# Performance work log

Hardware: AMD Instinct MI355X
Metric: run time of the kernel (lower is better)

Reference implementation:

```python
import jax, jax.numpy as jnp
import numpy as np

D = 1024      # in_features
H = 768       # hidden_features per routed expert
E = 8         # n_routed_experts
K = 2         # n_activated_experts
NS = 2        # n_shared_experts
ROUTE_SCALE = 1.0


def setup_inputs() -> dict:
    key = jax.random.key(0)
    ks = jax.random.split(key, 6)
    s = 0.02
    return {
        "x": jax.random.normal(ks[0], (2, 1024, D), jnp.float32),
        "gate_w": jax.random.normal(ks[1], (E, D), jnp.float32) * s,
        "W1": jax.random.normal(ks[2], (E, 2 * H, D), jnp.float32) * s,   # expert fc1 (y|gate)
        "W2": jax.random.normal(ks[3], (E, D, H), jnp.float32) * s,       # expert fc2
        "Ws1": jax.random.normal(ks[4], (2 * NS * H, D), jnp.float32) * s,  # shared fc1
        "Ws2": jax.random.normal(ks[5], (D, NS * H), jnp.float32) * s,      # shared fc2
    }


def _gated_mlp(x, w1, w2):
    # GatedMLP: fc1 -> chunk(2) -> y * silu(gate) -> fc2, all bias-free
    h = x @ w1.T
    y, g = jnp.split(h, 2, axis=-1)
    return (y * jax.nn.silu(g)) @ w2.T


def reference(x, gate_w, W1, W2, Ws1, Ws2):
    x_shape = x.shape
    xf = x.reshape(-1, D)                 # [T, D]
    T = xf.shape[0]

    # --- Gate: softmax scores in fp32, top-k routing ---
    scores = jax.nn.softmax((xf @ gate_w.T).astype(jnp.float32), axis=-1)  # [T, E]
    top_vals, top_idx = jax.lax.top_k(scores, K)
    # no bias branch (in_features != 7168): gathered original scores == top_k values
    weights = (top_vals * ROUTE_SCALE).astype(x.dtype)                      # [T, K]

    # Dense per-token/expert combine weights (0 for unselected experts);
    # mathematically identical to the per-expert gather/scatter-add combine.
    w_dense = jnp.zeros((T, E), x.dtype).at[jnp.arange(T)[:, None], top_idx].set(weights)

    # --- Routed experts (stacked GatedMLPs) ---
    h = jnp.einsum('td,ehd->teh', xf, W1)        # [T, E, 2H]
    y, g = jnp.split(h, 2, axis=-1)
    eo = jnp.einsum('teh,edh->ted', y * jax.nn.silu(g), W2)  # [T, E, D]
    z = jnp.einsum('te,ted->td', w_dense, eo)    # weighted combine

    # --- Shared experts ---
    z = z + _gated_mlp(xf, Ws1, Ws2)
    return z.reshape(x_shape)
```

## Files before the change

### kernel.cpp

```cpp
#include <hip/hip_runtime.h>
#include <hip/hip_bf16.h>


typedef short bf16x8 __attribute__((ext_vector_type(8)));
typedef float f32x4 __attribute__((ext_vector_type(4)));

__device__ __forceinline__ unsigned short f2b(float f) {
    __hip_bfloat16 h = __float2bfloat16(f);
    return *reinterpret_cast<unsigned short*>(&h);
}

__device__ __forceinline__ void ldst16(const unsigned short* g, unsigned short* l) {
    __builtin_amdgcn_global_load_lds(
        (const __attribute__((address_space(1))) unsigned int*)g,
        (__attribute__((address_space(3))) unsigned int*)l, 16, 0, 0);
}

__device__ __forceinline__ void cvt8(const float* s, unsigned short* d, int j) {
    const float4* sp = reinterpret_cast<const float4*>(s) + (size_t)j * 2;
    float4 v0 = sp[0], v1 = sp[1];
    union { unsigned short u[8]; uint4 v; } o;
    o.u[0]=f2b(v0.x); o.u[1]=f2b(v0.y); o.u[2]=f2b(v0.z); o.u[3]=f2b(v0.w);
    o.u[4]=f2b(v1.x); o.u[5]=f2b(v1.y); o.u[6]=f2b(v1.z); o.u[7]=f2b(v1.w);
    *(reinterpret_cast<uint4*>(d) + j) = o.v;
}

__global__ __launch_bounds__(256) void k_convgate(const float* __restrict__ x,
                                                  const float* __restrict__ gw,
                                                  const float* __restrict__ W1,
                                                  const float* __restrict__ Ws1,
                                                  const float* __restrict__ W2,
                                                  const float* __restrict__ Ws2,
                                                  unsigned short* __restrict__ xb,
                                                  unsigned short* __restrict__ W1b,
                                                  unsigned short* __restrict__ Ws1b,
                                                  unsigned short* __restrict__ W2b,
                                                  unsigned short* __restrict__ Ws2b,
                                                  int* __restrict__ tokslot,
                                                  float* __restrict__ wroute,
                                                  int* __restrict__ cnt,
                                                  float* __restrict__ out) {
    __shared__ float red[4][8];
    __shared__ float sc[8];
    const int b = blockIdx.x, tid = threadIdx.x;
    if (b < 11520) {
        int i = b * 256 + tid;
        if (i < 1572864)       cvt8(W1,  W1b,  i);
        else if (i < 1966080)  cvt8(Ws1, Ws1b, i - 1572864);
        else if (i < 2752512)  cvt8(W2,  W2b,  i - 1966080);
        else if (i < 2949120)  cvt8(Ws2, Ws2b, i - 2752512);
        return;
    }
    const int t = b - 11520;
    const int lane = tid & 63, w = tid >> 6;

    float4 v = reinterpret_cast<const float4*>(x + (size_t)t * 1024)[tid];
    union { unsigned short u[4]; } o;
    o.u[0]=f2b(v.x); o.u[1]=f2b(v.y); o.u[2]=f2b(v.z); o.u[3]=f2b(v.w);
    reinterpret_cast<ushort4*>(xb + (size_t)t * 1024)[tid] = *(ushort4*)o.u;

    float p[8];
    for (int e = 0; e < 8; e++) {
        float4 g = reinterpret_cast<const float4*>(gw + (size_t)e * 1024)[tid];
        p[e] = v.x*g.x + v.y*g.y + v.z*g.z + v.w*g.w;
    }
    for (int e = 0; e < 8; e++)
        for (int off = 32; off > 0; off >>= 1) p[e] += __shfl_down(p[e], off, 64);
    if (lane == 0)
        for (int e = 0; e < 8; e++) red[w][e] = p[e];
    __syncthreads();
    if (tid < 8) sc[tid] = red[0][tid] + red[1][tid] + red[2][tid] + red[3][tid];
    __syncthreads();
    if (tid == 0) {
        float m = sc[0];
        for (int e = 1; e < 8; e++) m = fmaxf(m, sc[e]);
        float ex[8], sum = 0.f;
        for (int e = 0; e < 8; e++) { ex[e] = expf(sc[e] - m); sum += ex[e]; }
        float inv = 1.f / sum;
        int i1 = 0;
        for (int e = 1; e < 8; e++) if (sc[e] > sc[i1]) i1 = e;
        int i2 = -1; float s2 = -1e30f;
        for (int e = 0; e < 8; e++) if (e != i1 && sc[e] > s2) { s2 = sc[e]; i2 = e; }
        int p1 = atomicAdd(&cnt[i1 * 16], 1);
        tokslot[i1 * 2048 + p1] = t; wroute[i1 * 2048 + p1] = ex[i1] * inv;
        int p2 = atomicAdd(&cnt[i2 * 16], 1);
        tokslot[i2 * 2048 + p2] = t; wroute[i2 * 2048 + p2] = ex[i2] * inv;
    }
    reinterpret_cast<float4*>(out + (size_t)t * 1024)[tid] = (float4){0.f, 0.f, 0.f, 0.f};
}

__global__ __launch_bounds__(256) void k_fc1u(const unsigned short* __restrict__ xb,
                                              const unsigned short* __restrict__ W1b,
                                              const unsigned short* __restrict__ Ws1b,
                                              const int* __restrict__ tokslot,
                                              const float* __restrict__ wroute,
                                              const int* __restrict__ cnt,
                                              unsigned short* __restrict__ act_r,
                                              unsigned short* __restrict__ acts) {
    __shared__ alignas(16) unsigned short As[128 * 64];
    __shared__ alignas(16) unsigned short Bs[128 * 64];
    const int tid = threadIdx.x, lane = tid & 63, w = tid >> 6;
    const int wr = w >> 1, wc = w & 1;
    const int mt = blockIdx.x / 12, ht = blockIdx.x % 12;

    int pre = 0, sel = -1, base = 0;
    for (int ee = 0; ee < 10; ee++) {
        int til = (ee < 8) ? ((cnt[ee * 16] + 127) >> 7) : 16;
        if (sel < 0 && mt < pre + til) { sel = ee; base = pre; }
        pre += til;
    }
    if (sel < 0) return;
    const int e = sel, m0 = (mt - base) * 128, h0 = ht * 64;
    const int Te = (e < 8) ? cnt[e * 16] : 2048;
    const unsigned short* Bp = (e < 8) ? (W1b + (size_t)e * 1536 * 1024)
                                       : (Ws1b + (size_t)(e - 8) * 768 * 1024);
    const int gOff = (e < 8) ? 768 : 1536;

    const int kc = tid & 7;
    int aoff[4], boff[4];
    for (int q = 0; q < 4; q++) {
        int row = q * 32 + (tid >> 3);
        int idx = m0 + row;
        int tk = (e < 8) ? ((idx < Te) ? tokslot[e * 2048 + idx] : 0) : idx;
        aoff[q] = tk * 1024 + ((kc ^ (row & 7)) << 3);
        int grow = (row < 64) ? (h0 + row) : (gOff + h0 + row - 64);
        boff[q] = grow * 1024 + ((kc ^ (row & 7)) << 3);
    }

    f32x4 accy[4][2], accg[4][2];
    for (int i = 0; i < 4; i++)
        for (int j = 0; j < 2; j++) {
            accy[i][j] = (f32x4){0.f, 0.f, 0.f, 0.f};
            accg[i][j] = (f32x4){0.f, 0.f, 0.f, 0.f};
        }

    for (int k0 = 0; k0 < 1024; k0 += 64) {
        for (int q = 0; q < 4; q++) {
            ldst16(xb + aoff[q] + k0, As + (q * 256 + tid) * 8);
            ldst16(Bp + boff[q] + k0, Bs + (q * 256 + tid) * 8);
        }
        __syncthreads();
        for (int kh = 0; kh < 2; kh++) {
            const int cq = kh * 4 + (lane >> 4);
            bf16x8 a[4], by[2], bg[2];
            for (int i = 0; i < 4; i++) {
                int r = 64 * wr + 16 * i + (lane & 15);
                a[i] = *(const bf16x8*)&As[r * 64 + ((cq ^ (r & 7)) << 3)];
            }
            for (int j = 0; j < 2; j++) {
                int ry = 32 * wc + 16 * j + (lane & 15);
                by[j] = *(const bf16x8*)&Bs[ry * 64 + ((cq ^ (ry & 7)) << 3)];
                int rg = 64 + ry;
                bg[j] = *(const bf16x8*)&Bs[rg * 64 + ((cq ^ (rg & 7)) << 3)];
            }
            for (int i = 0; i < 4; i++)
                for (int j = 0; j < 2; j++) {
                    accy[i][j] = __builtin_amdgcn_mfma_f32_16x16x32_bf16(a[i], by[j], accy[i][j], 0, 0, 0);
                    accg[i][j] = __builtin_amdgcn_mfma_f32_16x16x32_bf16(a[i], bg[j], accg[i][j], 0, 0, 0);
                }
        }
        __syncthreads();
    }

    for (int i = 0; i < 4; i++)
        for (int r = 0; r < 4; r++) {
            int irow = m0 + 64 * wr + 16 * i + ((lane >> 4) << 2) + r;
            if (irow >= Te) continue;
            float sw = (e < 8) ? wroute[e * 2048 + irow] : 1.0f;
            unsigned short* dst = (e < 8)
                ? (act_r + ((size_t)e * 2048 + irow) * 768)
                : (acts + (size_t)irow * 1536 + (size_t)(e - 8) * 768);
            for (int j = 0; j < 2; j++) {
                float y = accy[i][j][r], g = accg[i][j][r];
                float sg = g / (1.0f + __expf(-g));
                int col = h0 + 32 * wc + 16 * j + (lane & 15);
                dst[col] = f2b(sw * y * sg);
            }
        }
}

__global__ __launch_bounds__(256) void k_fc2u(const unsigned short* __restrict__ act_r,
                                              const unsigned short* __restrict__ acts,
                                              const unsigned short* __restrict__ W2b,
                                              const unsigned short* __restrict__ Ws2b,
                                              const int* __restrict__ tokslot,
                                              const int* __restrict__ cnt,
                                              float* __restrict__ out) {
    __shared__ alignas(16) unsigned short As[128 * 128];
    __shared__ alignas(16) unsigned short Bs[64 * 128];
    const int tid = threadIdx.x, lane = tid & 63, w = tid >> 6;
    const int wr = w >> 1, wc = w & 1;
    const int mt = blockIdx.x >> 4, nt = blockIdx.x & 15;

    int pre = 0, sel = -1, base = 0;
    for (int ee = 0; ee < 9; ee++) {
        int til = (ee < 8) ? ((cnt[ee * 16] + 127) >> 7) : 16;
        if (sel < 0 && mt < pre + til) { sel = ee; base = pre; }
        pre += til;
    }
    if (sel < 0) return;
    const int e = sel, m0 = (mt - base) * 128, n0 = nt * 64;
    int Te, astride, bstride, K;
    const unsigned short *Ab, *Bb;
    if (e < 8) {
        Te = cnt[e * 16]; K = 768; astride = 768; bstride = 768;
        Ab = act_r + (size_t)e * 2048 * 768;
        Bb = W2b + (size_t)e * 1024 * 768;
    } else {
        Te = 2048; K = 1536; astride = 1536; bstride = 1536;
        Ab = acts;
        Bb = Ws2b;
    }

    const int cp = tid & 15;
    int aoff[8], boff[4];
    for (int q = 0; q < 8; q++) {
        int row = q * 16 + (tid >> 4);
        aoff[q] = (m0 + row) * astride + ((cp ^ (row & 15)) << 3);
    }
    for (int q = 0; q < 4; q++) {
        int row = q * 16 + (tid >> 4);
        boff[q] = (n0 + row) * bstride + ((cp ^ (row & 15)) << 3);
    }

    f32x4 acc[4][2];
    for (int i = 0; i < 4; i++)
        for (int j = 0; j < 2; j++) acc[i][j] = (f32x4){0.f, 0.f, 0.f, 0.f};

    for (int k0 = 0; k0 < K; k0 += 128) {
        for (int q = 0; q < 8; q++) ldst16(Ab + aoff[q] + k0, As + (q * 256 + tid) * 8);
        for (int q = 0; q < 4; q++) ldst16(Bb + boff[q] + k0, Bs + (q * 256 + tid) * 8);
        __syncthreads();
        for (int kh = 0; kh < 4; kh++) {
            const int cq = kh * 4 + (lane >> 4);
            bf16x8 a[4], b[2];
            for (int i = 0; i < 4; i++) {
                int r = 64 * wr + 16 * i + (lane & 15);
                a[i] = *(const bf16x8*)&As[r * 128 + ((cq ^ (r & 15)) << 3)];
            }
            for (int j = 0; j < 2; j++) {
                int rb = 32 * wc + 16 * j + (lane & 15);
                b[j] = *(const bf16x8*)&Bs[rb * 128 + ((cq ^ (rb & 15)) << 3)];
            }
            for (int i = 0; i < 4; i++)
                for (int j = 0; j < 2; j++)
                    acc[i][j] = __builtin_amdgcn_mfma_f32_16x16x32_bf16(a[i], b[j], acc[i][j], 0, 0, 0);
        }
        __syncthreads();
    }

    for (int i = 0; i < 4; i++)
        for (int r = 0; r < 4; r++) {
            int irow = m0 + 64 * wr + 16 * i + ((lane >> 4) << 2) + r;
            if (irow >= Te) continue;
            int t = (e < 8) ? tokslot[e * 2048 + irow] : irow;
            for (int j = 0; j < 2; j++) {
                int col = n0 + 32 * wc + 16 * j + (lane & 15);
                atomicAdd(out + (size_t)t * 1024 + col, acc[i][j][r]);
            }
        }
}

extern "C" void kernel_launch(void* const* d_in, const int* in_sizes, int n_in,
                              void* d_out, int out_size, void* d_ws, size_t ws_size,
                              hipStream_t stream) {
    const float* x   = (const float*)d_in[0];
    const float* gw  = (const float*)d_in[1];
    const float* W1  = (const float*)d_in[2];
    const float* W2  = (const float*)d_in[3];
    const float* Ws1 = (const float*)d_in[4];
    const float* Ws2 = (const float*)d_in[5];
    float* out = (float*)d_out;

    char* ws = (char*)d_ws;
    unsigned short* xb    = (unsigned short*)(ws + 0);
    unsigned short* W1b   = (unsigned short*)(ws + 4194304);
    unsigned short* Ws1b  = (unsigned short*)(ws + 29360128);
    unsigned short* W2b   = (unsigned short*)(ws + 35651584);
    unsigned short* Ws2b  = (unsigned short*)(ws + 48234496);
    unsigned short* act_r = (unsigned short*)(ws + 51380224);
    unsigned short* acts  = (unsigned short*)(ws + 76546048);
    int*            tokslot = (int*)(ws + 82837504);
    float*          wroute  = (float*)(ws + 82903040);
    int*            cnt     = (int*)(ws + 82968576);

    hipMemsetAsync(cnt, 0, 512, stream);
    k_convgate<<<13568, 256, 0, stream>>>(x, gw, W1, Ws1, W2, Ws2,
                                          xb, W1b, Ws1b, W2b, Ws2b,
                                          tokslot, wroute, cnt, out);
    k_fc1u<<<864, 256, 0, stream>>>(xb, W1b, Ws1b, tokslot, wroute, cnt, act_r, acts);
    k_fc2u<<<896, 256, 0, stream>>>(act_r, acts, W2b, Ws2b, tokslot, cnt, out);
}
```

Before: 235.1 us.

## Double-buffer LDS tiles with 2-wave blocks and larger per-wave tiles in expert GEMMs

Both fc1 and fc2 GEMMs now use 128-thread blocks with two waves. Each wave computes a larger output sub-tile: 64x64 y/gate in fc1, and 64x128 in fc2, where the N tile grows to 128 and the grid is halved. K-slices shrink to 32 and are double-buffered in LDS, so the next slice's global-to-LDS load overlaps the current MFMAs, and one barrier per iteration replaces two. Shared-expert tiles are scheduled first so the heavier work starts early. The larger accumulators raise register pressure, and having fewer threads per block may reduce latency hiding.

```diff
diff --git a/kernel.cpp b/kernel.cpp
--- a/kernel.cpp
+++ b/kernel.cpp
@@ -89,7 +89,7 @@
     reinterpret_cast<float4*>(out + (size_t)t * 1024)[tid] = (float4){0.f, 0.f, 0.f, 0.f};
 }
 
-__global__ __launch_bounds__(256) void k_fc1u(const unsigned short* __restrict__ xb,
+__global__ __launch_bounds__(128) void k_fc1u(const unsigned short* __restrict__ xb,
                                               const unsigned short* __restrict__ W1b,
                                               const unsigned short* __restrict__ Ws1b,
                                               const int* __restrict__ tokslot,
@@ -97,166 +97,191 @@
                                               const int* __restrict__ cnt,
                                               unsigned short* __restrict__ act_r,
                                               unsigned short* __restrict__ acts) {
-    __shared__ alignas(16) unsigned short As[128 * 64];
-    __shared__ alignas(16) unsigned short Bs[128 * 64];
+    __shared__ alignas(16) unsigned short As[2][128 * 32];
+    __shared__ alignas(16) unsigned short Bs[2][128 * 32];
     const int tid = threadIdx.x, lane = tid & 63, w = tid >> 6;
-    const int wr = w >> 1, wc = w & 1;
     const int mt = blockIdx.x / 12, ht = blockIdx.x % 12;
-
-    int pre = 0, sel = -1, base = 0;
-    for (int ee = 0; ee < 10; ee++) {
-        int til = (ee < 8) ? ((cnt[ee * 16] + 127) >> 7) : 16;
-        if (sel < 0 && mt < pre + til) { sel = ee; base = pre; }
-        pre += til;
-    }
-    if (sel < 0) return;
-    const int e = sel, m0 = (mt - base) * 128, h0 = ht * 64;
+    const int h0 = ht * 64;
+
+    int e, m0;
+    if (mt < 32) { e = 8 + (mt >> 4); m0 = (mt & 15) * 128; }
+    else {
+        int rmt = mt - 32;
+        int pre = 0, sel = -1, base = 0;
+        for (int ee = 0; ee < 8; ee++) {
+            int til = (cnt[ee * 16] + 127) >> 7;
+            if (sel < 0 && rmt < pre + til) { sel = ee; base = pre; }
+            pre += til;
+        }
+        if (sel < 0) return;
+        e = sel; m0 = (rmt - base) * 128;
+    }
     const int Te = (e < 8) ? cnt[e * 16] : 2048;
     const unsigned short* Bp = (e < 8) ? (W1b + (size_t)e * 1536 * 1024)
                                        : (Ws1b + (size_t)(e - 8) * 768 * 1024);
     const int gOff = (e < 8) ? 768 : 1536;
 
-    const int kc = tid & 7;
     int aoff[4], boff[4];
     for (int q = 0; q < 4; q++) {
-        int row = q * 32 + (tid >> 3);
+        int row = q * 32 + (tid >> 2);
+        int p = tid & 3;
+        int sw = (row & 3) ^ ((row >> 2) & 3);
+        int ko = ((p ^ sw) << 3);
         int idx = m0 + row;
         int tk = (e < 8) ? ((idx < Te) ? tokslot[e * 2048 + idx] : 0) : idx;
-        aoff[q] = tk * 1024 + ((kc ^ (row & 7)) << 3);
+        aoff[q] = tk * 1024 + ko;
         int grow = (row < 64) ? (h0 + row) : (gOff + h0 + row - 64);
-        boff[q] = grow * 1024 + ((kc ^ (row & 7)) << 3);
-    }
-
-    f32x4 accy[4][2], accg[4][2];
+        boff[q] = grow * 1024 + ko;
+    }
+
+    f32x4 accy[4][4], accg[4][4];
     for (int i = 0; i < 4; i++)
-        for (int j = 0; j < 2; j++) {
+        for (int j = 0; j < 4; j++) {
             accy[i][j] = (f32x4){0.f, 0.f, 0.f, 0.f};
             accg[i][j] = (f32x4){0.f, 0.f, 0.f, 0.f};
         }
 
-    for (int k0 = 0; k0 < 1024; k0 += 64) {
-        for (int q = 0; q < 4; q++) {
-            ldst16(xb + aoff[q] + k0, As + (q * 256 + tid) * 8);
-            ldst16(Bp + boff[q] + k0, Bs + (q * 256 + tid) * 8);
-        }
+    for (int q = 0; q < 4; q++) {
+        ldst16(xb + aoff[q], &As[0][(q * 128 + tid) * 8]);
+        ldst16(Bp + boff[q], &Bs[0][(q * 128 + tid) * 8]);
+    }
+
+    const int cq = lane >> 4, lm = lane & 15;
+    for (int it = 0; it < 32; it++) {
+        const int bsel = it & 1;
         __syncthreads();
-        for (int kh = 0; kh < 2; kh++) {
-            const int cq = kh * 4 + (lane >> 4);
-            bf16x8 a[4], by[2], bg[2];
-            for (int i = 0; i < 4; i++) {
-                int r = 64 * wr + 16 * i + (lane & 15);
-                a[i] = *(const bf16x8*)&As[r * 64 + ((cq ^ (r & 7)) << 3)];
-            }
-            for (int j = 0; j < 2; j++) {
-                int ry = 32 * wc + 16 * j + (lane & 15);
-                by[j] = *(const bf16x8*)&Bs[ry * 64 + ((cq ^ (ry & 7)) << 3)];
-                int rg = 64 + ry;
-                bg[j] = *(const bf16x8*)&Bs[rg * 64 + ((cq ^ (rg & 7)) << 3)];
-            }
-            for (int i = 0; i < 4; i++)
-                for (int j = 0; j < 2; j++) {
-                    accy[i][j] = __builtin_amdgcn_mfma_f32_16x16x32_bf16(a[i], by[j], accy[i][j], 0, 0, 0);
-                    accg[i][j] = __builtin_amdgcn_mfma_f32_16x16x32_bf16(a[i], bg[j], accg[i][j], 0, 0, 0);
-                }
-        }
-        __syncthreads();
+        if (it + 1 < 32) {
+            int k0 = (it + 1) * 32, nb = bsel ^ 1;
+            for (int q = 0; q < 4; q++) {
+                ldst16(xb + aoff[q] + k0, &As[nb][(q * 128 + tid) * 8]);
+                ldst16(Bp + boff[q] + k0, &Bs[nb][(q * 128 + tid) * 8]);
+            }
+        }
+        bf16x8 a[4], by[4], bg[4];
+        for (int i = 0; i < 4; i++) {
+            int r = 64 * w + 16 * i + lm;
+            int s = (r & 3) ^ ((r >> 2) & 3);
+            a[i] = *(const bf16x8*)&As[bsel][r * 32 + ((cq ^ s) << 3)];
+        }
+        for (int j = 0; j < 4; j++) {
+            int r = 16 * j + lm;
+            int s = (r & 3) ^ ((r >> 2) & 3);
+            by[j] = *(const bf16x8*)&Bs[bsel][r * 32 + ((cq ^ s) << 3)];
+            int rg = 64 + r;
+            int s2 = (rg & 3) ^ ((rg >> 2) & 3);
+            bg[j] = *(const bf16x8*)&Bs[bsel][rg * 32 + ((cq ^ s2) << 3)];
+        }
+        for (int i = 0; i < 4; i++)
+            for (int j = 0; j < 4; j++) {
+                accy[i][j] = __builtin_amdgcn_mfma_f32_16x16x32_bf16(a[i], by[j], accy[i][j], 0, 0, 0);
+                accg[i][j] = __builtin_amdgcn_mfma_f32_16x16x32_bf16(a[i], bg[j], accg[i][j], 0, 0, 0);
+            }
     }
 
     for (int i = 0; i < 4; i++)
-        for (int r = 0; r < 4; r++) {
-            int irow = m0 + 64 * wr + 16 * i + ((lane >> 4) << 2) + r;
+        for (int r2 = 0; r2 < 4; r2++) {
+            int irow = m0 + 64 * w + 16 * i + ((lane >> 4) << 2) + r2;
             if (irow >= Te) continue;
-            float sw = (e < 8) ? wroute[e * 2048 + irow] : 1.0f;
+            float swt = (e < 8) ? wroute[e * 2048 + irow] : 1.0f;
             unsigned short* dst = (e < 8)
                 ? (act_r + ((size_t)e * 2048 + irow) * 768)
                 : (acts + (size_t)irow * 1536 + (size_t)(e - 8) * 768);
-            for (int j = 0; j < 2; j++) {
-                float y = accy[i][j][r], g = accg[i][j][r];
+            for (int j = 0; j < 4; j++) {
+                float y = accy[i][j][r2], g = accg[i][j][r2];
                 float sg = g / (1.0f + __expf(-g));
-                int col = h0 + 32 * wc + 16 * j + (lane & 15);
-                dst[col] = f2b(sw * y * sg);
-            }
-        }
-}
-
-__global__ __launch_bounds__(256) void k_fc2u(const unsigned short* __restrict__ act_r,
+                dst[h0 + 16 * j + lm] = f2b(swt * y * sg);
+            }
+        }
+}
+
+__global__ __launch_bounds__(128) void k_fc2u(const unsigned short* __restrict__ act_r,
                                               const unsigned short* __restrict__ acts,
                                               const unsigned short* __restrict__ W2b,
                                               const unsigned short* __restrict__ Ws2b,
                                               const int* __restrict__ tokslot,
                                               const int* __restrict__ cnt,
                                               float* __restrict__ out) {
-    __shared__ alignas(16) unsigned short As[128 * 128];
-    __shared__ alignas(16) unsigned short Bs[64 * 128];
+    __shared__ alignas(16) unsigned short As[2][128 * 32];
+    __shared__ alignas(16) unsigned short Bs[2][128 * 32];
     const int tid = threadIdx.x, lane = tid & 63, w = tid >> 6;
-    const int wr = w >> 1, wc = w & 1;
-    const int mt = blockIdx.x >> 4, nt = blockIdx.x & 15;
-
-    int pre = 0, sel = -1, base = 0;
-    for (int ee = 0; ee < 9; ee++) {
-        int til = (ee < 8) ? ((cnt[ee * 16] + 127) >> 7) : 16;
-        if (sel < 0 && mt < pre + til) { sel = ee; base = pre; }
-        pre += til;
-    }
-    if (sel < 0) return;
-    const int e = sel, m0 = (mt - base) * 128, n0 = nt * 64;
-    int Te, astride, bstride, K;
+    const int mt = blockIdx.x >> 3, nt = blockIdx.x & 7;
+    const int n0 = nt * 128;
+
+    int e, m0, K, astride, bstride, Te;
     const unsigned short *Ab, *Bb;
-    if (e < 8) {
-        Te = cnt[e * 16]; K = 768; astride = 768; bstride = 768;
+    if (mt < 16) {
+        e = 8; m0 = mt * 128; K = 1536; astride = 1536; bstride = 1536; Te = 2048;
+        Ab = acts; Bb = Ws2b;
+    } else {
+        int rmt = mt - 16;
+        int pre = 0, sel = -1, base = 0;
+        for (int ee = 0; ee < 8; ee++) {
+            int til = (cnt[ee * 16] + 127) >> 7;
+            if (sel < 0 && rmt < pre + til) { sel = ee; base = pre; }
+            pre += til;
+        }
+        if (sel < 0) return;
+        e = sel; m0 = (rmt - base) * 128; K = 768; astride = 768; bstride = 768;
+        Te = cnt[e * 16];
         Ab = act_r + (size_t)e * 2048 * 768;
         Bb = W2b + (size_t)e * 1024 * 768;
-    } else {
-        Te = 2048; K = 1536; astride = 1536; bstride = 1536;
-        Ab = acts;
-        Bb = Ws2b;
-    }
-
-    const int cp = tid & 15;
-    int aoff[8], boff[4];
-    for (int q = 0; q < 8; q++) {
-        int row = q * 16 + (tid >> 4);
-        aoff[q] = (m0 + row) * astride + ((cp ^ (row & 15)) << 3);
-    }
+    }
+
+    int aoff[4], boff[4];
     for (int q = 0; q < 4; q++) {
-        int row = q * 16 + (tid >> 4);
-        boff[q] = (n0 + row) * bstride + ((cp ^ (row & 15)) << 3);
-    }
-
-    f32x4 acc[4][2];
+        int row = q * 32 + (tid >> 2);
+        int p = tid & 3;
+        int sw = (row & 3) ^ ((row >> 2) & 3);
+        int ko = ((p ^ sw) << 3);
+        aoff[q] = (m0 + row) * astride + ko;
+        boff[q] = (n0 + row) * bstride + ko;
+    }
+
+    f32x4 acc[4][8];
     for (int i = 0; i < 4; i++)
-        for (int j = 0; j < 2; j++) acc[i][j] = (f32x4){0.f, 0.f, 0.f, 0.f};
-
-    for (int k0 = 0; k0 < K; k0 += 128) {
-        for (int q = 0; q < 8; q++) ldst16(Ab + aoff[q] + k0, As + (q * 256 + tid) * 8);
-        for (int q = 0; q < 4; q++) ldst16(Bb + boff[q] + k0, Bs + (q * 256 + tid) * 8);
+        for (int j = 0; j < 8; j++) acc[i][j] = (f32x4){0.f, 0.f, 0.f, 0.f};
+
+    for (int q = 0; q < 4; q++) {
+        ldst16(Ab + aoff[q], &As[0][(q * 128 + tid) * 8]);
+        ldst16(Bb + boff[q], &Bs[0][(q * 128 + tid) * 8]);
+    }
+
+    const int cq = lane >> 4, lm = lane & 15;
+    const int niter = K >> 5;
+    for (int it = 0; it < niter; it++) {
+        const int bsel = it & 1;
         __syncthreads();
-        for (int kh = 0; kh < 4; kh++) {
-            const int cq = kh * 4 + (lane >> 4);
-            bf16x8 a[4], b[2];
-            for (int i = 0; i < 4; i++) {
-                int r = 64 * wr + 16 * i + (lane & 15);
-                a[i] = *(const bf16x8*)&As[r * 128 + ((cq ^ (r & 15)) << 3)];
-            }
-            for (int j = 0; j < 2; j++) {
-                int rb = 32 * wc + 16 * j + (lane & 15);
-                b[j] = *(const bf16x8*)&Bs[rb * 128 + ((cq ^ (rb & 15)) << 3)];
-            }
-            for (int i = 0; i < 4; i++)
-                for (int j = 0; j < 2; j++)
-                    acc[i][j] = __builtin_amdgcn_mfma_f32_16x16x32_bf16(a[i], b[j], acc[i][j], 0, 0, 0);
-        }
-        __syncthreads();
+        if (it + 1 < niter) {
+            int k0 = (it + 1) * 32, nb = bsel ^ 1;
+            for (int q = 0; q < 4; q++) {
+                ldst16(Ab + aoff[q] + k0, &As[nb][(q * 128 + tid) * 8]);
+                ldst16(Bb + boff[q] + k0, &Bs[nb][(q * 128 + tid) * 8]);
+            }
+        }
+        bf16x8 a[4], bfr[8];
+        for (int i = 0; i < 4; i++) {
+            int r = 64 * w + 16 * i + lm;
+            int s = (r & 3) ^ ((r >> 2) & 3);
+            a[i] = *(const bf16x8*)&As[bsel][r * 32 + ((cq ^ s) << 3)];
+        }
+        for (int j = 0; j < 8; j++) {
+            int r = 16 * j + lm;
+            int s = (r & 3) ^ ((r >> 2) & 3);
+            bfr[j] = *(const bf16x8*)&Bs[bsel][r * 32 + ((cq ^ s) << 3)];
+        }
+        for (int i = 0; i < 4; i++)
+            for (int j = 0; j < 8; j++)
+                acc[i][j] = __builtin_amdgcn_mfma_f32_16x16x32_bf16(a[i], bfr[j], acc[i][j], 0, 0, 0);
     }
 
     for (int i = 0; i < 4; i++)
-        for (int r = 0; r < 4; r++) {
-            int irow = m0 + 64 * wr + 16 * i + ((lane >> 4) << 2) + r;
+        for (int r2 = 0; r2 < 4; r2++) {
+            int irow = m0 + 64 * w + 16 * i + ((lane >> 4) << 2) + r2;
             if (irow >= Te) continue;
             int t = (e < 8) ? tokslot[e * 2048 + irow] : irow;
-            for (int j = 0; j < 2; j++) {
-                int col = n0 + 32 * wc + 16 * j + (lane & 15);
-                atomicAdd(out + (size_t)t * 1024 + col, acc[i][j][r]);
+            for (int j = 0; j < 8; j++) {
+                int col = n0 + 16 * j + lm;
+                atomicAdd(out + (size_t)t * 1024 + col, acc[i][j][r2]);
             }
         }
 }
@@ -288,6 +313,6 @@
     k_convgate<<<13568, 256, 0, stream>>>(x, gw, W1, Ws1, W2, Ws2,
                                           xb, W1b, Ws1b, W2b, Ws2b,
                                           tokslot, wroute, cnt, out);
-    k_fc1u<<<864, 256, 0, stream>>>(xb, W1b, Ws1b, tokslot, wroute, cnt, act_r, acts);
-    k_fc2u<<<896, 256, 0, stream>>>(act_r, acts, W2b, Ws2b, tokslot, cnt, out);
-}
+    k_fc1u<<<864, 128, 0, stream>>>(xb, W1b, Ws1b, tokslot, wroute, cnt, act_r, acts);
+    k_fc2u<<<448, 128, 0, stream>>>(act_r, acts, W2b, Ws2b, tokslot, cnt, out);
+}
```

Result: slower. 301.1 us (+28.1%).

## Shrink GEMM K-tiles, batch weight conversion per block, schedule shared fc2 first

Applied to the files above, without the earlier changes.

The weight-conversion blocks now each handle four chunks, cutting the conversion grid from 11520 to 2880 blocks. The fc1 K-tile shrinks from 64 to 32 and the fc2 K-tile from 128 to 64, with the LDS swizzle patterns reworked to match, so each block uses less shared memory and more blocks can be resident per CU. In fc2 the shared-expert tiles, which have the longest K, are moved to the first block indices so they start early and leave the shorter routed tiles to fill in at the end. Smaller K-tiles mean twice as many barriers and load rounds per GEMM, with less work between each sync.

```diff
diff --git a/kernel.cpp b/kernel.cpp
--- a/kernel.cpp
+++ b/kernel.cpp
@@ -43,15 +43,17 @@
     __shared__ float red[4][8];
     __shared__ float sc[8];
     const int b = blockIdx.x, tid = threadIdx.x;
-    if (b < 11520) {
-        int i = b * 256 + tid;
-        if (i < 1572864)       cvt8(W1,  W1b,  i);
-        else if (i < 1966080)  cvt8(Ws1, Ws1b, i - 1572864);
-        else if (i < 2752512)  cvt8(W2,  W2b,  i - 1966080);
-        else if (i < 2949120)  cvt8(Ws2, Ws2b, i - 2752512);
+    if (b < 2880) {
+        for (int q = 0; q < 4; q++) {
+            int i = b * 1024 + q * 256 + tid;
+            if (i < 1572864)       cvt8(W1,  W1b,  i);
+            else if (i < 1966080)  cvt8(Ws1, Ws1b, i - 1572864);
+            else if (i < 2752512)  cvt8(W2,  W2b,  i - 1966080);
+            else                   cvt8(Ws2, Ws2b, i - 2752512);
+        }
         return;
     }
-    const int t = b - 11520;
+    const int t = b - 2880;
     const int lane = tid & 63, w = tid >> 6;
 
     float4 v = reinterpret_cast<const float4*>(x + (size_t)t * 1024)[tid];
@@ -97,11 +99,12 @@
                                               const int* __restrict__ cnt,
                                               unsigned short* __restrict__ act_r,
                                               unsigned short* __restrict__ acts) {
-    __shared__ alignas(16) unsigned short As[128 * 64];
-    __shared__ alignas(16) unsigned short Bs[128 * 64];
+    __shared__ alignas(16) unsigned short As[128 * 32];
+    __shared__ alignas(16) unsigned short Bs[128 * 32];
     const int tid = threadIdx.x, lane = tid & 63, w = tid >> 6;
     const int wr = w >> 1, wc = w & 1;
     const int mt = blockIdx.x / 12, ht = blockIdx.x % 12;
+    const int h0 = ht * 64;
 
     int pre = 0, sel = -1, base = 0;
     for (int ee = 0; ee < 10; ee++) {
@@ -110,21 +113,22 @@
         pre += til;
     }
     if (sel < 0) return;
-    const int e = sel, m0 = (mt - base) * 128, h0 = ht * 64;
+    const int e = sel, m0 = (mt - base) * 128;
     const int Te = (e < 8) ? cnt[e * 16] : 2048;
     const unsigned short* Bp = (e < 8) ? (W1b + (size_t)e * 1536 * 1024)
                                        : (Ws1b + (size_t)(e - 8) * 768 * 1024);
     const int gOff = (e < 8) ? 768 : 1536;
 
-    const int kc = tid & 7;
-    int aoff[4], boff[4];
-    for (int q = 0; q < 4; q++) {
-        int row = q * 32 + (tid >> 3);
+    int aoff[2], boff[2];
+    for (int q = 0; q < 2; q++) {
+        int ch = q * 256 + tid;
+        int row = ch >> 2, c = ch & 3;
+        int ko = ((c ^ ((row >> 1) & 3)) << 3);
         int idx = m0 + row;
         int tk = (e < 8) ? ((idx < Te) ? tokslot[e * 2048 + idx] : 0) : idx;
-        aoff[q] = tk * 1024 + ((kc ^ (row & 7)) << 3);
+        aoff[q] = tk * 1024 + ko;
         int grow = (row < 64) ? (h0 + row) : (gOff + h0 + row - 64);
-        boff[q] = grow * 1024 + ((kc ^ (row & 7)) << 3);
+        boff[q] = grow * 1024 + ko;
     }
 
     f32x4 accy[4][2], accg[4][2];
@@ -134,47 +138,44 @@
             accg[i][j] = (f32x4){0.f, 0.f, 0.f, 0.f};
         }
 
-    for (int k0 = 0; k0 < 1024; k0 += 64) {
-        for (int q = 0; q < 4; q++) {
+    const int cq = lane >> 4, lm = lane & 15;
+    for (int k0 = 0; k0 < 1024; k0 += 32) {
+        for (int q = 0; q < 2; q++) {
             ldst16(xb + aoff[q] + k0, As + (q * 256 + tid) * 8);
             ldst16(Bp + boff[q] + k0, Bs + (q * 256 + tid) * 8);
         }
         __syncthreads();
-        for (int kh = 0; kh < 2; kh++) {
-            const int cq = kh * 4 + (lane >> 4);
-            bf16x8 a[4], by[2], bg[2];
-            for (int i = 0; i < 4; i++) {
-                int r = 64 * wr + 16 * i + (lane & 15);
-                a[i] = *(const bf16x8*)&As[r * 64 + ((cq ^ (r & 7)) << 3)];
-            }
-            for (int j = 0; j < 2; j++) {
-                int ry = 32 * wc + 16 * j + (lane & 15);
-                by[j] = *(const bf16x8*)&Bs[ry * 64 + ((cq ^ (ry & 7)) << 3)];
-                int rg = 64 + ry;
-                bg[j] = *(const bf16x8*)&Bs[rg * 64 + ((cq ^ (rg & 7)) << 3)];
-            }
-            for (int i = 0; i < 4; i++)
-                for (int j = 0; j < 2; j++) {
-                    accy[i][j] = __builtin_amdgcn_mfma_f32_16x16x32_bf16(a[i], by[j], accy[i][j], 0, 0, 0);
-                    accg[i][j] = __builtin_amdgcn_mfma_f32_16x16x32_bf16(a[i], bg[j], accg[i][j], 0, 0, 0);
-                }
-        }
-        __syncthreads();
-    }
-
-    for (int i = 0; i < 4; i++)
-        for (int r = 0; r < 4; r++) {
-            int irow = m0 + 64 * wr + 16 * i + ((lane >> 4) << 2) + r;
+        bf16x8 a[4], by[2], bg[2];
+        for (int i = 0; i < 4; i++) {
+            int r = 64 * wr + 16 * i + lm;
+            a[i] = *(const bf16x8*)&As[r * 32 + ((cq ^ ((r >> 1) & 3)) << 3)];
+        }
+        for (int j = 0; j < 2; j++) {
+            int ry = 32 * wc + 16 * j + lm;
+            by[j] = *(const bf16x8*)&Bs[ry * 32 + ((cq ^ ((ry >> 1) & 3)) << 3)];
+            int rg = 64 + ry;
+            bg[j] = *(const bf16x8*)&Bs[rg * 32 + ((cq ^ ((rg >> 1) & 3)) << 3)];
+        }
+        for (int i = 0; i < 4; i++)
+            for (int j = 0; j < 2; j++) {
+                accy[i][j] = __builtin_amdgcn_mfma_f32_16x16x32_bf16(a[i], by[j], accy[i][j], 0, 0, 0);
+                accg[i][j] = __builtin_amdgcn_mfma_f32_16x16x32_bf16(a[i], bg[j], accg[i][j], 0, 0, 0);
+            }
+        __syncthreads();
+    }
+
+    for (int i = 0; i < 4; i++)
+        for (int r2 = 0; r2 < 4; r2++) {
+            int irow = m0 + 64 * wr + 16 * i + ((lane >> 4) << 2) + r2;
             if (irow >= Te) continue;
             float sw = (e < 8) ? wroute[e * 2048 + irow] : 1.0f;
             unsigned short* dst = (e < 8)
                 ? (act_r + ((size_t)e * 2048 + irow) * 768)
                 : (acts + (size_t)irow * 1536 + (size_t)(e - 8) * 768);
             for (int j = 0; j < 2; j++) {
-                float y = accy[i][j][r], g = accg[i][j][r];
+                float y = accy[i][j][r2], g = accg[i][j][r2];
                 float sg = g / (1.0f + __expf(-g));
-                int col = h0 + 32 * wc + 16 * j + (lane & 15);
-                dst[col] = f2b(sw * y * sg);
+                dst[h0 + 32 * wc + 16 * j + lm] = f2b(sw * y * sg);
             }
         }
 }
@@ -186,61 +187,64 @@
                                               const int* __restrict__ tokslot,
                                               const int* __restrict__ cnt,
                                               float* __restrict__ out) {
-    __shared__ alignas(16) unsigned short As[128 * 128];
-    __shared__ alignas(16) unsigned short Bs[64 * 128];
+    __shared__ alignas(16) unsigned short As[128 * 64];
+    __shared__ alignas(16) unsigned short Bs[64 * 64];
     const int tid = threadIdx.x, lane = tid & 63, w = tid >> 6;
     const int wr = w >> 1, wc = w & 1;
     const int mt = blockIdx.x >> 4, nt = blockIdx.x & 15;
-
-    int pre = 0, sel = -1, base = 0;
-    for (int ee = 0; ee < 9; ee++) {
-        int til = (ee < 8) ? ((cnt[ee * 16] + 127) >> 7) : 16;
-        if (sel < 0 && mt < pre + til) { sel = ee; base = pre; }
-        pre += til;
-    }
-    if (sel < 0) return;
-    const int e = sel, m0 = (mt - base) * 128, n0 = nt * 64;
-    int Te, astride, bstride, K;
+    const int n0 = nt * 64;
+
+    int e, m0, K, astride, bstride, Te;
     const unsigned short *Ab, *Bb;
-    if (e < 8) {
-        Te = cnt[e * 16]; K = 768; astride = 768; bstride = 768;
+    if (mt < 16) {
+        e = 8; m0 = mt * 128; K = 1536; astride = 1536; bstride = 1536; Te = 2048;
+        Ab = acts; Bb = Ws2b;
+    } else {
+        int rmt = mt - 16;
+        int pre = 0, sel = -1, base = 0;
+        for (int ee = 0; ee < 8; ee++) {
+            int til = (cnt[ee * 16] + 127) >> 7;
+            if (sel < 0 && rmt < pre + til) { sel = ee; base = pre; }
+            pre += til;
+        }
+        if (sel < 0) return;
+        e = sel; m0 = (rmt - base) * 128; K = 768; astride = 768; bstride = 768;
+        Te = cnt[e * 16];
         Ab = act_r + (size_t)e * 2048 * 768;
         Bb = W2b + (size_t)e * 1024 * 768;
-    } else {
-        Te = 2048; K = 1536; astride = 1536; bstride = 1536;
-        Ab = acts;
-        Bb = Ws2b;
-    }
-
-    const int cp = tid & 15;
-    int aoff[8], boff[4];
-    for (int q = 0; q < 8; q++) {
-        int row = q * 16 + (tid >> 4);
-        aoff[q] = (m0 + row) * astride + ((cp ^ (row & 15)) << 3);
-    }
+    }
+
+    int aoff[4], boff[2];
     for (int q = 0; q < 4; q++) {
-        int row = q * 16 + (tid >> 4);
-        boff[q] = (n0 + row) * bstride + ((cp ^ (row & 15)) << 3);
+        int ch = q * 256 + tid;
+        int row = ch >> 3, c = ch & 7;
+        aoff[q] = (m0 + row) * astride + ((c ^ (row & 7)) << 3);
+    }
+    for (int q = 0; q < 2; q++) {
+        int ch = q * 256 + tid;
+        int row = ch >> 3, c = ch & 7;
+        boff[q] = (n0 + row) * bstride + ((c ^ (row & 7)) << 3);
     }
 
     f32x4 acc[4][2];
     for (int i = 0; i < 4; i++)
         for (int j = 0; j < 2; j++) acc[i][j] = (f32x4){0.f, 0.f, 0.f, 0.f};
 
-    for (int k0 = 0; k0 < K; k0 += 128) {
-        for (int q = 0; q < 8; q++) ldst16(Ab + aoff[q] + k0, As + (q * 256 + tid) * 8);
-        for (int q = 0; q < 4; q++) ldst16(Bb + boff[q] + k0, Bs + (q * 256 + tid) * 8);
-        __syncthreads();
-        for (int kh = 0; kh < 4; kh++) {
+    const int lm = lane & 15;
+    for (int k0 = 0; k0 < K; k0 += 64) {
+        for (int q = 0; q < 4; q++) ldst16(Ab + aoff[q] + k0, As + (q * 256 + tid) * 8);
+        for (int q = 0; q < 2; q++) ldst16(Bb + boff[q] + k0, Bs + (q * 256 + tid) * 8);
+        __syncthreads();
+        for (int kh = 0; kh < 2; kh++) {
             const int cq = kh * 4 + (lane >> 4);
             bf16x8 a[4], b[2];
             for (int i = 0; i < 4; i++) {
-                int r = 64 * wr + 16 * i + (lane & 15);
-                a[i] = *(const bf16x8*)&As[r * 128 + ((cq ^ (r & 15)) << 3)];
-            }
-            for (int j = 0; j < 2; j++) {
-                int rb = 32 * wc + 16 * j + (lane & 15);
-                b[j] = *(const bf16x8*)&Bs[rb * 128 + ((cq ^ (rb & 15)) << 3)];
+                int r = 64 * wr + 16 * i + lm;
+                a[i] = *(const bf16x8*)&As[r * 64 + ((cq ^ (r & 7)) << 3)];
+            }
+            for (int j = 0; j < 2; j++) {
+                int rb = 32 * wc + 16 * j + lm;
+                b[j] = *(const bf16x8*)&Bs[rb * 64 + ((cq ^ (rb & 7)) << 3)];
             }
             for (int i = 0; i < 4; i++)
                 for (int j = 0; j < 2; j++)
@@ -250,13 +254,13 @@
     }
 
     for (int i = 0; i < 4; i++)
-        for (int r = 0; r < 4; r++) {
-            int irow = m0 + 64 * wr + 16 * i + ((lane >> 4) << 2) + r;
+        for (int r2 = 0; r2 < 4; r2++) {
+            int irow = m0 + 64 * wr + 16 * i + ((lane >> 4) << 2) + r2;
             if (irow >= Te) continue;
             int t = (e < 8) ? tokslot[e * 2048 + irow] : irow;
             for (int j = 0; j < 2; j++) {
-                int col = n0 + 32 * wc + 16 * j + (lane & 15);
-                atomicAdd(out + (size_t)t * 1024 + col, acc[i][j][r]);
+                int col = n0 + 32 * wc + 16 * j + lm;
+                atomicAdd(out + (size_t)t * 1024 + col, acc[i][j][r2]);
             }
         }
 }
@@ -285,9 +289,9 @@
     int*            cnt     = (int*)(ws + 82968576);
 
     hipMemsetAsync(cnt, 0, 512, stream);
-    k_convgate<<<13568, 256, 0, stream>>>(x, gw, W1, Ws1, W2, Ws2,
-                                          xb, W1b, Ws1b, W2b, Ws2b,
-                                          tokslot, wroute, cnt, out);
+    k_convgate<<<4928, 256, 0, stream>>>(x, gw, W1, Ws1, W2, Ws2,
+                                         xb, W1b, Ws1b, W2b, Ws2b,
+                                         tokslot, wroute, cnt, out);
     k_fc1u<<<864, 256, 0, stream>>>(xb, W1b, Ws1b, tokslot, wroute, cnt, act_r, acts);
     k_fc2u<<<896, 256, 0, stream>>>(act_r, acts, W2b, Ws2b, tokslot, cnt, out);
 }
```

After: 237.6 us. Within noise of the previous version (+1.1%).
